# Kernel optimization log

Hardware: AMD Instinct MI355X
Metric: run time of the kernel (lower is better)

Reference implementation:

```python
import jax, jax.numpy as jnp
import numpy as np

N_NODES = 100000
N_EDGES = 640000
DIM = 128
N_LAYERS = 3

def setup_inputs() -> dict:
    key = jax.random.key(0)
    k1, k2, k3 = jax.random.split(key, 3)
    x = jax.random.normal(k1, (1, N_NODES, DIM), dtype=jnp.float32)
    edge_index = jax.random.randint(k2, (2, N_EDGES), 0, N_NODES, dtype=jnp.int64)
    Ws = jax.random.normal(k3, (N_LAYERS, DIM, DIM), dtype=jnp.float32) * (1.0 / np.sqrt(DIM))
    bs = jnp.zeros((N_LAYERS, DIM), dtype=jnp.float32)
    return {"x": x, "edge_index": edge_index, "Ws": Ws, "bs": bs}

def reference(x, edge_index, Ws, bs):
    # Stacked PyG-style GCNConv layers with ReLU, as in GraphEncoder (gnn_type='gcn').
    # GCNConv: add self-loops, symmetric norm D^-1/2 A D^-1/2, h W, scatter-sum, + bias.
    h = x[0]                                  # [N, D] (squeeze batch dim of 1)
    N = h.shape[0]
    loops = jnp.arange(N, dtype=edge_index.dtype)
    src = jnp.concatenate([edge_index[0], loops])   # [E+N] message sources
    dst = jnp.concatenate([edge_index[1], loops])   # [E+N] aggregation targets
    deg = jax.ops.segment_sum(jnp.ones_like(dst, dtype=h.dtype), dst, num_segments=N)
    dinv = jnp.where(deg > 0, jax.lax.rsqrt(deg), 0.0)
    norm = (dinv[src] * dinv[dst])[:, None]         # [E+N, 1] edge weights
    for l in range(Ws.shape[0]):
        m = norm * (h @ Ws[l])[src]                 # gather + per-edge message
        h = jax.ops.segment_sum(m, dst, num_segments=N) + bs[l]
        h = jax.nn.relu(h)
    return h[None]                                  # [1, N, D]
```

## Files before the change

kernel.cpp:

```cpp
#include <hip/hip_runtime.h>

#define DIM 128

typedef unsigned int uint32;
typedef short bf16x8 __attribute__((ext_vector_type(8)));
typedef float f32x4 __attribute__((ext_vector_type(4)));

__device__ __forceinline__ unsigned short f2b(float f) {
    return (unsigned short)((__float_as_uint(f) + 0x8000u) >> 16);
}
__device__ __forceinline__ uint32 packbf2(float lo, float hi) {
    uint32 a = __float_as_uint(lo);
    uint32 b = __float_as_uint(hi);
    return ((a + 0x8000u) >> 16) | ((b + 0x8000u) & 0xffff0000u);
}
__device__ __forceinline__ float bflo(uint32 u) { return __uint_as_float(u << 16); }
__device__ __forceinline__ float bfhi(uint32 u) { return __uint_as_float(u & 0xffff0000u); }

__global__ __launch_bounds__(256) void k_count(const int* __restrict__ dst,
                                               int* __restrict__ cnt, int E) {
    int e = blockIdx.x * 256 + threadIdx.x;
    if (e < E) atomicAdd(&cnt[dst[e]], 1);
}

__global__ __launch_bounds__(256) void k_dinv(const int* __restrict__ cnt,
                                              float* __restrict__ dinv, int n) {
    int i = blockIdx.x * 256 + threadIdx.x;
    if (i < n) dinv[i] = rsqrtf((float)(cnt[i] + 1));
}

__global__ __launch_bounds__(256) void k_scaleg(const float* __restrict__ x,
                                                const float* __restrict__ dinv,
                                                uint32* __restrict__ g, int n) {
    int t = blockIdx.x * 256 + threadIdx.x;
    if (t >= n * 64) return;
    int node = t >> 6;
    float dv = dinv[node];
    float2 v = ((const float2*)x)[t];
    g[t] = packbf2(dv * v.x, dv * v.y);
}

__global__ __launch_bounds__(256) void k_scan1(const int* __restrict__ cnt,
                                               int* __restrict__ incl,
                                               int* __restrict__ bsums, int n) {
    __shared__ int tmp[256];
    int i = blockIdx.x * 256 + threadIdx.x;
    int t = threadIdx.x;
    tmp[t] = (i < n) ? cnt[i] : 0;
    __syncthreads();
#pragma unroll
    for (int off = 1; off < 256; off <<= 1) {
        int v = (t >= off) ? tmp[t - off] : 0;
        __syncthreads();
        tmp[t] += v;
        __syncthreads();
    }
    if (i < n) incl[i] = tmp[t];
    if (t == 255) bsums[blockIdx.x] = tmp[255];
}

__global__ __launch_bounds__(512) void k_scan2(int* __restrict__ bsums, int nb) {
    __shared__ int tmp[512];
    int t = threadIdx.x;
    tmp[t] = (t < nb) ? bsums[t] : 0;
    __syncthreads();
#pragma unroll
    for (int off = 1; off < 512; off <<= 1) {
        int v = (t >= off) ? tmp[t - off] : 0;
        __syncthreads();
        tmp[t] += v;
        __syncthreads();
    }
    if (t < nb) bsums[t] = (t == 0) ? 0 : tmp[t - 1];
}

__global__ __launch_bounds__(256) void k_scan3(int* __restrict__ incl,
                                               const int* __restrict__ bsums, int n) {
    int i = blockIdx.x * 256 + threadIdx.x;
    if (i < n) incl[i] += bsums[blockIdx.x];
}

__global__ __launch_bounds__(256) void k_fill(const int* __restrict__ src,
                                              const int* __restrict__ dst,
                                              int* __restrict__ incl,
                                              int* __restrict__ srcs, int E) {
    int e = blockIdx.x * 256 + threadIdx.x;
    if (e >= E) return;
    int p = atomicSub(&incl[dst[e]], 1) - 1;
    srcs[p] = src[e];
}

__global__ __launch_bounds__(256) void k_prepW(const float* __restrict__ Ws,
                                               short* __restrict__ Wb, int total) {
    int t = blockIdx.x * 256 + threadIdx.x;
    if (t >= total) return;
    int layer = t >> 14;
    int idx = t & 16383;
    int j = idx & 7;
    int l = (idx >> 3) & 63;
    int f = idx >> 9;
    int ks = f & 3;
    int cs = (f >> 2) & 1;
    int w = f >> 3;
    int nn = w * 32 + cs * 16 + (l & 15);
    int kk = ks * 32 + (l >> 4) * 8 + j;
    Wb[t] = (short)f2b(Ws[(size_t)layer * DIM * DIM + kk * DIM + nn]);
}

__global__ __launch_bounds__(256) void k_aggregate(const uint32* __restrict__ g,
                                                   const int* __restrict__ srcs,
                                                   const int* __restrict__ rowptr,
                                                   const float* __restrict__ dinv,
                                                   uint32* __restrict__ m, int n, int E) {
    int tid = threadIdx.x;
    int node = blockIdx.x * 8 + ((tid >> 6) << 1) + ((tid >> 5) & 1);
    if (node >= n) return;
    int sub = tid & 31;
    int start = rowptr[node];
    int end = (node + 1 < n) ? rowptr[node + 1] : E;

    const uint2* g2 = (const uint2*)g;
    uint2 us = g2[(size_t)node * 32 + sub];
    float a0 = bflo(us.x), a1 = bfhi(us.x), a2 = bflo(us.y), a3 = bfhi(us.y);

    int p = start;
    for (; p + 4 <= end; p += 4) {
        int s0 = srcs[p + 0];
        int s1 = srcs[p + 1];
        int s2 = srcs[p + 2];
        int s3 = srcs[p + 3];
        uint2 u0 = g2[(size_t)s0 * 32 + sub];
        uint2 u1 = g2[(size_t)s1 * 32 + sub];
        uint2 u2 = g2[(size_t)s2 * 32 + sub];
        uint2 u3 = g2[(size_t)s3 * 32 + sub];
        a0 += bflo(u0.x) + bflo(u1.x) + bflo(u2.x) + bflo(u3.x);
        a1 += bfhi(u0.x) + bfhi(u1.x) + bfhi(u2.x) + bfhi(u3.x);
        a2 += bflo(u0.y) + bflo(u1.y) + bflo(u2.y) + bflo(u3.y);
        a3 += bfhi(u0.y) + bfhi(u1.y) + bfhi(u2.y) + bfhi(u3.y);
    }
    for (; p < end; ++p) {
        uint2 u = g2[(size_t)srcs[p] * 32 + sub];
        a0 += bflo(u.x);
        a1 += bfhi(u.x);
        a2 += bflo(u.y);
        a3 += bfhi(u.y);
    }

    float di = dinv[node];
    uint2 o;
    o.x = packbf2(di * a0, di * a1);
    o.y = packbf2(di * a2, di * a3);
    ((uint2*)m)[(size_t)node * 32 + sub] = o;
}

__global__ __launch_bounds__(256) void k_gemm_mfma(const unsigned short* __restrict__ M,
                                                   const short* __restrict__ Wb,
                                                   const float* __restrict__ dinv,
                                                   const float* __restrict__ bias,
                                                   unsigned short* __restrict__ Gn,
                                                   float* __restrict__ Out,
                                                   int n, int final_layer) {
    int tid = threadIdx.x;
    int w = tid >> 6;
    int l = tid & 63;
    int lr = l & 15;
    int lg = l >> 4;
    int row0 = blockIdx.x * 32;

    const bf16x8* wb = (const bf16x8*)Wb;
    bf16x8 bfrag[2][4];
#pragma unroll
    for (int cs = 0; cs < 2; ++cs)
#pragma unroll
        for (int ks = 0; ks < 4; ++ks)
            bfrag[cs][ks] = wb[((w * 2 + cs) * 4 + ks) * 64 + l];

    f32x4 acc[2][2];
#pragma unroll
    for (int rs = 0; rs < 2; ++rs)
#pragma unroll
        for (int cs = 0; cs < 2; ++cs) acc[rs][cs] = (f32x4){0.f, 0.f, 0.f, 0.f};

    int r0 = row0 + lr;
    int r1 = row0 + 16 + lr;
    bool ok0 = r0 < n, ok1 = r1 < n;
    const unsigned short* m0 = M + (size_t)r0 * DIM + lg * 8;
    const unsigned short* m1 = M + (size_t)r1 * DIM + lg * 8;

    const bf16x8 zf = (bf16x8){0, 0, 0, 0, 0, 0, 0, 0};
#pragma unroll
    for (int ks = 0; ks < 4; ++ks) {
        bf16x8 a0 = ok0 ? *(const bf16x8*)(m0 + ks * 32) : zf;
        bf16x8 a1 = ok1 ? *(const bf16x8*)(m1 + ks * 32) : zf;
#pragma unroll
        for (int cs = 0; cs < 2; ++cs) {
            acc[0][cs] = __builtin_amdgcn_mfma_f32_16x16x32_bf16(a0, bfrag[cs][ks], acc[0][cs], 0, 0, 0);
            acc[1][cs] = __builtin_amdgcn_mfma_f32_16x16x32_bf16(a1, bfrag[cs][ks], acc[1][cs], 0, 0, 0);
        }
    }

    float b0 = bias[w * 32 + lr];
    float b1 = bias[w * 32 + 16 + lr];

#pragma unroll
    for (int rs = 0; rs < 2; ++rs)
#pragma unroll
        for (int r = 0; r < 4; ++r) {
            int grow = row0 + rs * 16 + lg * 4 + r;
            if (grow < n) {
                float h0 = fmaxf(acc[rs][0][r] + b0, 0.f);
                float h1 = fmaxf(acc[rs][1][r] + b1, 0.f);
                if (final_layer) {
                    Out[(size_t)grow * DIM + w * 32 + lr]      = h0;
                    Out[(size_t)grow * DIM + w * 32 + 16 + lr] = h1;
                } else {
                    float dv = dinv[grow];
                    Gn[(size_t)grow * DIM + w * 32 + lr]      = f2b(dv * h0);
                    Gn[(size_t)grow * DIM + w * 32 + 16 + lr] = f2b(dv * h1);
                }
            }
        }
}

extern "C" void kernel_launch(void* const* d_in, const int* in_sizes, int n_in,
                              void* d_out, int out_size, void* d_ws, size_t ws_size,
                              hipStream_t stream) {
    const float* x  = (const float*)d_in[0];
    const int*   ei = (const int*)d_in[1];
    const float* Ws = (const float*)d_in[2];
    const float* bs = (const float*)d_in[3];

    const int N = in_sizes[0] / DIM;
    const int E = in_sizes[1] / 2;
    const int L = in_sizes[2] / (DIM * DIM);

    const int* src = ei;
    const int* dst = ei + E;

    float* out = (float*)d_out;

    char* ws = (char*)d_ws;
    uint32* g    = (uint32*)ws;                ws += (size_t)N * 64 * 4;
    uint32* m    = (uint32*)ws;                ws += (size_t)N * 64 * 4;
    short* Wb    = (short*)ws;                 ws += (size_t)L * 16384 * 2;
    float* dinv  = (float*)ws;                 ws += (size_t)N * 4;
    int*   cnt   = (int*)ws;                   ws += (size_t)N * 4;
    int*   incl  = (int*)ws;                   ws += (size_t)N * 4;
    int*   srcs  = (int*)ws;                   ws += (size_t)E * 4;
    int*   bsums = (int*)ws;                   ws += 512 * 4;

    const int nbN = (N + 255) / 256;
    const int nbE = (E + 255) / 256;
    const int totW = L * 16384;

    k_prepW<<<(totW + 255) / 256, 256, 0, stream>>>(Ws, Wb, totW);
    hipMemsetAsync(cnt, 0, (size_t)N * 4, stream);
    k_count<<<nbE, 256, 0, stream>>>(dst, cnt, E);
    k_dinv <<<nbN, 256, 0, stream>>>(cnt, dinv, N);
    k_scaleg<<<(N * 64 + 255) / 256, 256, 0, stream>>>(x, dinv, g, N);
    k_scan1<<<nbN, 256, 0, stream>>>(cnt, incl, bsums, N);
    k_scan2<<<1, 512, 0, stream>>>(bsums, nbN);
    k_scan3<<<nbN, 256, 0, stream>>>(incl, bsums, N);
    k_fill <<<nbE, 256, 0, stream>>>(src, dst, incl, srcs, E);

    for (int l = 0; l < L; ++l) {
        k_aggregate<<<(N + 7) / 8, 256, 0, stream>>>(g, srcs, incl, dinv, m, N, E);
        k_gemm_mfma<<<(N + 31) / 32, 256, 0, stream>>>((const unsigned short*)m,
                                                       Wb + (size_t)l * 16384, dinv,
                                                       bs + (size_t)l * DIM,
                                                       (unsigned short*)g, out,
                                                       N, l == L - 1);
    }
}
```

Baseline: 353.1 us.

## Fuse neighbor aggregation and MFMA GEMM into one per-layer kernel via LDS

Aggregation and the bf16 MFMA transform now run in a single kernel per layer. Each block gathers 32 node rows into padded shared memory and multiplies them by W directly, with ping-pong feature buffers between layers. This removes the global write and re-read of the intermediate aggregate matrix and one launch per layer. The dinv computation is also folded into the first scan kernel. In exchange, each block has fewer independent gather streams (4 nodes per half-wave, serialized) and must pass a barrier before the MFMA step, which can reduce latency hiding for the irregular gathers.

```diff
diff --git a/kernel.cpp b/kernel.cpp
--- a/kernel.cpp
+++ b/kernel.cpp
@@ -1,6 +1,7 @@
 #include <hip/hip_runtime.h>
 
 #define DIM 128
+#define MROW 272
 
 typedef unsigned int uint32;
 typedef short bf16x8 __attribute__((ext_vector_type(8)));
@@ -21,12 +22,6 @@
                                                int* __restrict__ cnt, int E) {
     int e = blockIdx.x * 256 + threadIdx.x;
     if (e < E) atomicAdd(&cnt[dst[e]], 1);
-}
-
-__global__ __launch_bounds__(256) void k_dinv(const int* __restrict__ cnt,
-                                              float* __restrict__ dinv, int n) {
-    int i = blockIdx.x * 256 + threadIdx.x;
-    if (i < n) dinv[i] = rsqrtf((float)(cnt[i] + 1));
 }
 
 __global__ __launch_bounds__(256) void k_scaleg(const float* __restrict__ x,
@@ -42,11 +37,14 @@
 
 __global__ __launch_bounds__(256) void k_scan1(const int* __restrict__ cnt,
                                                int* __restrict__ incl,
-                                               int* __restrict__ bsums, int n) {
+                                               int* __restrict__ bsums,
+                                               float* __restrict__ dinv, int n) {
     __shared__ int tmp[256];
     int i = blockIdx.x * 256 + threadIdx.x;
     int t = threadIdx.x;
-    tmp[t] = (i < n) ? cnt[i] : 0;
+    int c = (i < n) ? cnt[i] : 0;
+    if (i < n) dinv[i] = rsqrtf((float)(c + 1));
+    tmp[t] = c;
     __syncthreads();
 #pragma unroll
     for (int off = 1; off < 256; off <<= 1) {
@@ -107,65 +105,22 @@
     Wb[t] = (short)f2b(Ws[(size_t)layer * DIM * DIM + kk * DIM + nn]);
 }
 
-__global__ __launch_bounds__(256) void k_aggregate(const uint32* __restrict__ g,
-                                                   const int* __restrict__ srcs,
-                                                   const int* __restrict__ rowptr,
-                                                   const float* __restrict__ dinv,
-                                                   uint32* __restrict__ m, int n, int E) {
+__global__ __launch_bounds__(256) void k_layer(const uint32* __restrict__ g,
+                                               const int* __restrict__ srcs,
+                                               const int* __restrict__ rowptr,
+                                               const float* __restrict__ dinv,
+                                               const short* __restrict__ Wb,
+                                               const float* __restrict__ bias,
+                                               uint32* __restrict__ Gn,
+                                               float* __restrict__ Out,
+                                               int n, int E, int final_layer) {
+    __shared__ __align__(16) char smem[32 * MROW];
     int tid = threadIdx.x;
-    int node = blockIdx.x * 8 + ((tid >> 6) << 1) + ((tid >> 5) & 1);
-    if (node >= n) return;
-    int sub = tid & 31;
-    int start = rowptr[node];
-    int end = (node + 1 < n) ? rowptr[node + 1] : E;
-
-    const uint2* g2 = (const uint2*)g;
-    uint2 us = g2[(size_t)node * 32 + sub];
-    float a0 = bflo(us.x), a1 = bfhi(us.x), a2 = bflo(us.y), a3 = bfhi(us.y);
-
-    int p = start;
-    for (; p + 4 <= end; p += 4) {
-        int s0 = srcs[p + 0];
-        int s1 = srcs[p + 1];
-        int s2 = srcs[p + 2];
-        int s3 = srcs[p + 3];
-        uint2 u0 = g2[(size_t)s0 * 32 + sub];
-        uint2 u1 = g2[(size_t)s1 * 32 + sub];
-        uint2 u2 = g2[(size_t)s2 * 32 + sub];
-        uint2 u3 = g2[(size_t)s3 * 32 + sub];
-        a0 += bflo(u0.x) + bflo(u1.x) + bflo(u2.x) + bflo(u3.x);
-        a1 += bfhi(u0.x) + bfhi(u1.x) + bfhi(u2.x) + bfhi(u3.x);
-        a2 += bflo(u0.y) + bflo(u1.y) + bflo(u2.y) + bflo(u3.y);
-        a3 += bfhi(u0.y) + bfhi(u1.y) + bfhi(u2.y) + bfhi(u3.y);
-    }
-    for (; p < end; ++p) {
-        uint2 u = g2[(size_t)srcs[p] * 32 + sub];
-        a0 += bflo(u.x);
-        a1 += bfhi(u.x);
-        a2 += bflo(u.y);
-        a3 += bfhi(u.y);
-    }
-
-    float di = dinv[node];
-    uint2 o;
-    o.x = packbf2(di * a0, di * a1);
-    o.y = packbf2(di * a2, di * a3);
-    ((uint2*)m)[(size_t)node * 32 + sub] = o;
-}
-
-__global__ __launch_bounds__(256) void k_gemm_mfma(const unsigned short* __restrict__ M,
-                                                   const short* __restrict__ Wb,
-                                                   const float* __restrict__ dinv,
-                                                   const float* __restrict__ bias,
-                                                   unsigned short* __restrict__ Gn,
-                                                   float* __restrict__ Out,
-                                                   int n, int final_layer) {
-    int tid = threadIdx.x;
+    int row0 = blockIdx.x * 32;
     int w = tid >> 6;
     int l = tid & 63;
     int lr = l & 15;
     int lg = l >> 4;
-    int row0 = blockIdx.x * 32;
 
     const bf16x8* wb = (const bf16x8*)Wb;
     bf16x8 bfrag[2][4];
@@ -175,23 +130,61 @@
         for (int ks = 0; ks < 4; ++ks)
             bfrag[cs][ks] = wb[((w * 2 + cs) * 4 + ks) * 64 + l];
 
+    int hw = tid >> 5;
+    int sub = tid & 31;
+    const uint2* g2 = (const uint2*)g;
+#pragma unroll
+    for (int i = 0; i < 4; ++i) {
+        int nl = hw * 4 + i;
+        int node = row0 + nl;
+        uint2 o = make_uint2(0u, 0u);
+        if (node < n) {
+            int start = rowptr[node];
+            int end = (node + 1 < n) ? rowptr[node + 1] : E;
+            uint2 us = g2[(size_t)node * 32 + sub];
+            float a0 = bflo(us.x), a1 = bfhi(us.x), a2 = bflo(us.y), a3 = bfhi(us.y);
+            int p = start;
+            for (; p + 4 <= end; p += 4) {
+                int s0 = srcs[p + 0];
+                int s1 = srcs[p + 1];
+                int s2 = srcs[p + 2];
+                int s3 = srcs[p + 3];
+                uint2 u0 = g2[(size_t)s0 * 32 + sub];
+                uint2 u1 = g2[(size_t)s1 * 32 + sub];
+                uint2 u2 = g2[(size_t)s2 * 32 + sub];
+                uint2 u3 = g2[(size_t)s3 * 32 + sub];
+                a0 += bflo(u0.x) + bflo(u1.x) + bflo(u2.x) + bflo(u3.x);
+                a1 += bfhi(u0.x) + bfhi(u1.x) + bfhi(u2.x) + bfhi(u3.x);
+                a2 += bflo(u0.y) + bflo(u1.y) + bflo(u2.y) + bflo(u3.y);
+                a3 += bfhi(u0.y) + bfhi(u1.y) + bfhi(u2.y) + bfhi(u3.y);
+            }
+            for (; p < end; ++p) {
+                uint2 u = g2[(size_t)srcs[p] * 32 + sub];
+                a0 += bflo(u.x);
+                a1 += bfhi(u.x);
+                a2 += bflo(u.y);
+                a3 += bfhi(u.y);
+            }
+            float di = dinv[node];
+            o.x = packbf2(di * a0, di * a1);
+            o.y = packbf2(di * a2, di * a3);
+        }
+        *(uint2*)(smem + nl * MROW + sub * 8) = o;
+    }
+    __syncthreads();
+
     f32x4 acc[2][2];
 #pragma unroll
     for (int rs = 0; rs < 2; ++rs)
 #pragma unroll
         for (int cs = 0; cs < 2; ++cs) acc[rs][cs] = (f32x4){0.f, 0.f, 0.f, 0.f};
 
-    int r0 = row0 + lr;
-    int r1 = row0 + 16 + lr;
-    bool ok0 = r0 < n, ok1 = r1 < n;
-    const unsigned short* m0 = M + (size_t)r0 * DIM + lg * 8;
-    const unsigned short* m1 = M + (size_t)r1 * DIM + lg * 8;
-
-    const bf16x8 zf = (bf16x8){0, 0, 0, 0, 0, 0, 0, 0};
+    const char* base0 = smem + lr * MROW + lg * 16;
+    const char* base1 = smem + (16 + lr) * MROW + lg * 16;
 #pragma unroll
     for (int ks = 0; ks < 4; ++ks) {
-        bf16x8 a0 = ok0 ? *(const bf16x8*)(m0 + ks * 32) : zf;
-        bf16x8 a1 = ok1 ? *(const bf16x8*)(m1 + ks * 32) : zf;
+        bf16x8 a0 = *(const bf16x8*)(base0 + ks * 64);
+        bf16x8 a1 = *(const bf16x8*)(base1 + ks * 64);
 #pragma unroll
         for (int cs = 0; cs < 2; ++cs) {
             acc[0][cs] = __builtin_amdgcn_mfma_f32_16x16x32_bf16(a0, bfrag[cs][ks], acc[0][cs], 0, 0, 0);
@@ -215,8 +208,9 @@
                     Out[(size_t)grow * DIM + w * 32 + 16 + lr] = h1;
                 } else {
                     float dv = dinv[grow];
-                    Gn[(size_t)grow * DIM + w * 32 + lr]      = f2b(dv * h0);
-                    Gn[(size_t)grow * DIM + w * 32 + 16 + lr] = f2b(dv * h1);
+                    unsigned short* gp = (unsigned short*)Gn;
+                    gp[(size_t)grow * DIM + w * 32 + lr]      = f2b(dv * h0);
+                    gp[(size_t)grow * DIM + w * 32 + 16 + lr] = f2b(dv * h1);
                 }
             }
         }
@@ -240,8 +234,8 @@
     float* out = (float*)d_out;
 
     char* ws = (char*)d_ws;
-    uint32* g    = (uint32*)ws;                ws += (size_t)N * 64 * 4;
-    uint32* m    = (uint32*)ws;                ws += (size_t)N * 64 * 4;
+    uint32* g0   = (uint32*)ws;                ws += (size_t)N * 64 * 4;
+    uint32* g1   = (uint32*)ws;                ws += (size_t)N * 64 * 4;
     short* Wb    = (short*)ws;                 ws += (size_t)L * 16384 * 2;
     float* dinv  = (float*)ws;                 ws += (size_t)N * 4;
     int*   cnt   = (int*)ws;                   ws += (size_t)N * 4;
@@ -256,19 +250,20 @@
     k_prepW<<<(totW + 255) / 256, 256, 0, stream>>>(Ws, Wb, totW);
     hipMemsetAsync(cnt, 0, (size_t)N * 4, stream);
     k_count<<<nbE, 256, 0, stream>>>(dst, cnt, E);
-    k_dinv <<<nbN, 256, 0, stream>>>(cnt, dinv, N);
-    k_scaleg<<<(N * 64 + 255) / 256, 256, 0, stream>>>(x, dinv, g, N);
-    k_scan1<<<nbN, 256, 0, stream>>>(cnt, incl, bsums, N);
+    k_scan1<<<nbN, 256, 0, stream>>>(cnt, incl, bsums, dinv, N);
     k_scan2<<<1, 512, 0, stream>>>(bsums, nbN);
+    k_scaleg<<<(N * 64 + 255) / 256, 256, 0, stream>>>(x, dinv, g0, N);
     k_scan3<<<nbN, 256, 0, stream>>>(incl, bsums, N);
     k_fill <<<nbE, 256, 0, stream>>>(src, dst, incl, srcs, E);
 
+    const int nblk = (N + 31) / 32;
+    uint32* gin = g0;
     for (int l = 0; l < L; ++l) {
-        k_aggregate<<<(N + 7) / 8, 256, 0, stream>>>(g, srcs, incl, dinv, m, N, E);
-        k_gemm_mfma<<<(N + 31) / 32, 256, 0, stream>>>((const unsigned short*)m,
-                                                       Wb + (size_t)l * 16384, dinv,
-                                                       bs + (size_t)l * DIM,
-                                                       (unsigned short*)g, out,
-                                                       N, l == L - 1);
-    }
-}
+        uint32* gout = (gin == g0) ? g1 : g0;
+        k_layer<<<nblk, 256, 0, stream>>>(gin, srcs, incl, dinv,
+                                          Wb + (size_t)l * 16384,
+                                          bs + (size_t)l * DIM,
+                                          gout, out, N, E, l == L - 1);
+        gin = gout;
+    }
+}
```

Result: faster. 340.7 us (-3.5%).
